# Performance work log

Hardware: AMD Instinct MI355X
Metric: run time of the kernel (lower is better)

## Reference

```python
import jax, jax.numpy as jnp
import numpy as np

EPS = 1e-12
W_MAX = 0.8
ALPHA_MAX = 1.5
T = 10
ETA = 0.2
ALPHA_SCALE = 1.0
N = 50000
IN_DIM = 512
HID = 256
C = 8
EH = 64
E2 = 400000  # undirected pairs; E = 2*E2 directed edges


def setup_inputs() -> dict:
    key = jax.random.key(0)
    ks = jax.random.split(key, 12)
    x = jax.random.normal(ks[0], (N, IN_DIM), jnp.float32)
    src0 = jax.random.randint(ks[1], (E2,), 0, N)
    dst0 = jax.random.randint(ks[2], (E2,), 0, N)
    edge_index = jnp.concatenate([jnp.stack([src0, dst0]), jnp.stack([dst0, src0])], axis=1)
    rev = jnp.concatenate([jnp.arange(E2) + E2, jnp.arange(E2)])
    def lin(k, i, o):
        return jax.random.normal(k, (i, o), jnp.float32) * (2.0 / i) ** 0.5
    enc_w1 = lin(ks[3], IN_DIM, HID); enc_b1 = jnp.zeros((HID,), jnp.float32)
    enc_w2 = lin(ks[4], HID, C); enc_b2 = jnp.zeros((C,), jnp.float32)
    edge_w1 = lin(ks[5], 2 * HID + 2, EH); edge_b1 = jnp.zeros((EH,), jnp.float32)
    edge_w2 = lin(ks[6], EH, 1); edge_b2 = jnp.zeros((1,), jnp.float32)
    bound = (6.0 / (C + C)) ** 0.5  # xavier_uniform
    R_raw = jax.random.uniform(ks[7], (C, C), jnp.float32, -bound, bound) + 0.5 * jnp.eye(C, dtype=jnp.float32)
    R_scale_log = jnp.float32(0.0)
    msg_logit = jnp.float32(-3.0)
    return dict(x=x, edge_index=edge_index, rev=rev,
                enc_w1=enc_w1, enc_b1=enc_b1, enc_w2=enc_w2, enc_b2=enc_b2,
                edge_w1=edge_w1, edge_b1=edge_b1, edge_w2=edge_w2, edge_b2=edge_b2,
                R_raw=R_raw, R_scale_log=R_scale_log, msg_logit=msg_logit)


def reference(x, edge_index, rev, enc_w1, enc_b1, enc_w2, enc_b2,
              edge_w1, edge_b1, edge_w2, edge_b2, R_raw, R_scale_log, msg_logit):
    num_nodes = x.shape[0]
    src, dst = edge_index[0], edge_index[1]
    # unary encoder (mlp type, eval mode -> no dropout)
    h = jax.nn.relu(x @ enc_w1 + enc_b1)
    logits = h @ enc_w2 + enc_b2
    log_phi = jax.nn.log_softmax(logits, axis=-1)  # [N, C]
    # structural edge features from out-degree of src
    deg = jax.ops.segment_sum(jnp.ones_like(src, jnp.float32), src, num_segments=num_nodes)
    logdeg = jnp.log(deg + 1.0)
    a, b = logdeg[src], logdeg[dst]
    struct = jnp.stack([a + b, jnp.abs(a - b)], axis=-1)  # [E, 2]
    # learned symmetric edge weights -> per-edge kernel K
    hs, hd = h[src], h[dst]
    edge_in = jnp.concatenate([hs * hd, jnp.abs(hs - hd), struct], axis=-1)  # [E, 2H+2]
    eh = jax.nn.relu(edge_in @ edge_w1 + edge_b1)
    w_raw = (eh @ edge_w2 + edge_b2)[:, 0]
    w = W_MAX * jax.nn.sigmoid(w_raw)
    w = 0.5 * (w + w[rev])
    R = 0.5 * (R_raw + R_raw.T)
    R = (jax.nn.softplus(R_scale_log) + 1e-06) * jnp.tanh(R)
    K = jnp.exp(w[:, None, None] * R[None])  # [E, C, C]
    degc = jnp.maximum(deg, 1.0)
    edge_norm = (degc[src] * degc[dst]) ** -0.5  # [E]
    alpha = ALPHA_MAX * jax.nn.sigmoid(msg_logit) * ALPHA_SCALE
    lp_src = log_phi[src]
    m = jax.nn.softmax(lp_src, axis=-1)  # init_unary=True

    def step(m, _):
        f = jnp.einsum('ec,ecd->ed', m, K)
        log_f = jnp.log(jnp.maximum(f, EPS)) * edge_norm[:, None]
        sum_in = jax.ops.segment_sum(log_f, dst, num_segments=num_nodes)
        excl = sum_in[src] - log_f[rev]
        m_new = jax.nn.softmax(lp_src + alpha * excl, axis=-1)
        m = (1.0 - ETA) * m + ETA * m_new
        m = jnp.maximum(m, EPS)
        m = m / m.sum(axis=-1, keepdims=True)
        return m, None

    m, _ = jax.lax.scan(step, m, None, length=T)
    # beliefs
    f = jnp.einsum('ec,ecd->ed', m, K)
    log_f = jnp.log(jnp.maximum(f, EPS)) * edge_norm[:, None]
    sum_in = jax.ops.segment_sum(log_f, dst, num_segments=num_nodes)
    beliefs = jax.nn.softmax(log_phi + alpha * sum_in, axis=-1)
    return beliefs
```

## Files before the change

kernel.cpp:

```cpp
#include <hip/hip_runtime.h>
#include <cstddef>
#include <cstdint>

typedef _Float16 h4 __attribute__((ext_vector_type(4)));
typedef _Float16 h8 __attribute__((ext_vector_type(8)));
typedef float    f4 __attribute__((ext_vector_type(4)));

#define NN      50000
#define IND     512
#define HIDN    256
#define E2P     400000
#define EDD     800000
#define NBLK    196

#define OFF_HF16    ((size_t)0)
#define OFF_LOGF    ((size_t)0)
#define OFF_Z       ((size_t)25600000)
#define OFF_DEG     ((size_t)28800000)
#define OFF_LOGDEG  ((size_t)29000000)
#define OFF_DEGC    ((size_t)29200000)
#define OFF_BASE    ((size_t)29400000)
#define OFF_CNT     ((size_t)29600000)
#define OFF_BLK     ((size_t)29800000)
#define OFF_WT      ((size_t)29804096)
#define OFF_BT      ((size_t)30066240)
#define OFF_RS      ((size_t)30135872)
#define OFF_WSYM    ((size_t)30136384)
#define OFF_ENORM   ((size_t)31736384)
#define OFF_POS     ((size_t)33336384)
#define OFF_MA      ((size_t)36536384)
#define OFF_MB      ((size_t)49336384)
#define WS_NEED     ((size_t)62136384)

__global__ void k_deg(const int* __restrict__ ei, int* __restrict__ deg) {
    int e = blockIdx.x * 256 + threadIdx.x;
    atomicAdd(&deg[ei[e]], 1);
}

__global__ void k_node(const int* __restrict__ deg, float* __restrict__ logdeg,
                       float* __restrict__ degc) {
    int n = blockIdx.x * 256 + threadIdx.x;
    if (n < NN) {
        float d = (float)deg[n];
        logdeg[n] = logf(d + 1.0f);
        degc[n]   = fmaxf(d, 1.0f);
    }
}

__global__ void k_scan1(const int* __restrict__ deg, int* __restrict__ incl,
                        int* __restrict__ blk) {
    __shared__ int sm[256];
    int i = blockIdx.x * 256 + threadIdx.x;
    int v = (i < NN) ? deg[i] : 0;
    sm[threadIdx.x] = v;
    __syncthreads();
    for (int off = 1; off < 256; off <<= 1) {
        int t = (threadIdx.x >= off) ? sm[threadIdx.x - off] : 0;
        __syncthreads();
        sm[threadIdx.x] += t;
        __syncthreads();
    }
    if (i < NN) incl[i] = sm[threadIdx.x];
    if (threadIdx.x == 255) blk[blockIdx.x] = sm[255];
}

__global__ void k_scan2(int* __restrict__ blk) {
    __shared__ int sm[256];
    int v = (threadIdx.x < NBLK) ? blk[threadIdx.x] : 0;
    sm[threadIdx.x] = v;
    __syncthreads();
    for (int off = 1; off < 256; off <<= 1) {
        int t = (threadIdx.x >= off) ? sm[threadIdx.x - off] : 0;
        __syncthreads();
        sm[threadIdx.x] += t;
        __syncthreads();
    }
    if (threadIdx.x < NBLK) blk[threadIdx.x] = sm[threadIdx.x];
}

__global__ void k_scan3(const int* __restrict__ incl, const int* __restrict__ deg,
                        const int* __restrict__ blk, int* __restrict__ base) {
    int i = blockIdx.x * 256 + threadIdx.x;
    if (i < NN) {
        int off = (blockIdx.x > 0) ? blk[blockIdx.x - 1] : 0;
        base[i] = off + incl[i] - deg[i];
    }
}

__global__ void k_pos(const int* __restrict__ ei, const int* __restrict__ base,
                      int* __restrict__ cnt, int* __restrict__ pos) {
    int e = blockIdx.x * 256 + threadIdx.x;
    int dstn = ei[EDD + e];
    pos[e] = base[dstn] + atomicAdd(&cnt[dstn], 1);
}

__global__ void k_prep(const float* __restrict__ enc_w1, const float* __restrict__ edge_w1,
                       const float* __restrict__ R_raw, const float* __restrict__ Rsl,
                       const float* __restrict__ mlog,
                       _Float16* __restrict__ Wt, _Float16* __restrict__ Bt,
                       float* __restrict__ Rs) {
    int gid = blockIdx.x * 256 + threadIdx.x;
    if (gid < 256 * 512) {
        int n = gid >> 9, k = gid & 511;
        Wt[n * 512 + k] = (_Float16)enc_w1[k * 256 + n];
        return;
    }
    int g2 = gid - 256 * 512;
    if (g2 < 64 * 544) {
        int n = g2 / 544, k = g2 - n * 544;
        float v = 0.0f;
        if (k < 512) {
            int tm = k >> 5, r = k & 31;
            int qq = r >> 3, jj = (r >> 1) & 3, typ = k & 1;
            int c = (tm >> 1) * 32 + qq * 8 + (tm & 1) * 4 + jj;
            v = edge_w1[(typ ? 256 + c : c) * 64 + n];
        } else if (k < 514) {
            v = edge_w1[k * 64 + n];
        }
        Bt[n * 544 + k] = (_Float16)v;
        return;
    }
    int g3 = g2 - 64 * 544;
    if (g3 < 64) {
        int c = g3 >> 3, d = g3 & 7;
        float rv = 0.5f * (R_raw[c * 8 + d] + R_raw[d * 8 + c]);
        float s  = log1pf(expf(Rsl[0])) + 1e-6f;
        Rs[g3] = s * tanhf(rv);
        return;
    }
    if (g3 == 64) {
        Rs[64] = 1.5f / (1.0f + expf(-mlog[0]));
    }
}

__global__ __launch_bounds__(256) void k_enc(const float* __restrict__ x,
                                             const _Float16* __restrict__ Wt,
                                             const float* __restrict__ b1,
                                             _Float16* __restrict__ hf) {
    __shared__ _Float16 XL[64 * 40];
    __shared__ _Float16 WL[256 * 40];
    const int tid = threadIdx.x;
    const int wid = tid >> 6;
    const int lane = tid & 63;
    const int l15 = lane & 15;
    const int q = lane >> 4;
    const int m0 = blockIdx.x * 64;

    f4 acc[16];
#pragma unroll
    for (int i = 0; i < 16; i++) acc[i] = (f4){0.f, 0.f, 0.f, 0.f};

    const int xr = tid >> 2;
    const int xs = tid & 3;
    const int gr = m0 + xr;

    for (int kt = 0; kt < 16; kt++) {
        __syncthreads();
        f4 xv0 = (f4){0, 0, 0, 0}, xv1 = (f4){0, 0, 0, 0};
        if (gr < NN) {
            const f4* xp = (const f4*)(x + (size_t)gr * IND + kt * 32 + xs * 8);
            xv0 = xp[0]; xv1 = xp[1];
        }
        h8 xh;
#pragma unroll
        for (int u = 0; u < 4; u++) { xh[u] = (_Float16)xv0[u]; xh[4 + u] = (_Float16)xv1[u]; }
        *(h8*)&XL[xr * 40 + xs * 8] = xh;
#pragma unroll
        for (int rep = 0; rep < 4; rep++) {
            int cid = rep * 256 + tid;
            int n = cid >> 2;
            int off = (cid & 3) * 8;
            h8 wv = *(const h8*)(Wt + (size_t)n * IND + kt * 32 + off);
            *(h8*)&WL[n * 40 + off] = wv;
        }
        __syncthreads();
        h8 a = *(const h8*)&XL[(wid * 16 + l15) * 40 + q * 8];
#pragma unroll
        for (int nt = 0; nt < 16; nt++) {
            h8 b = *(const h8*)&WL[(nt * 16 + l15) * 40 + q * 8];
            acc[nt] = __builtin_amdgcn_mfma_f32_16x16x32_f16(a, b, acc[nt], 0, 0, 0);
        }
    }
#pragma unroll
    for (int nt = 0; nt < 16; nt++) {
        int col = nt * 16 + l15;
        float bv = b1[col];
#pragma unroll
        for (int reg = 0; reg < 4; reg++) {
            int row = m0 + wid * 16 + q * 4 + reg;
            if (row < NN) {
                float v = acc[nt][reg] + bv;
                hf[(size_t)row * HIDN + col] = (_Float16)fmaxf(v, 0.f);
            }
        }
    }
}

__global__ void k_logits(const _Float16* __restrict__ hf, const float* __restrict__ w2,
                         const float* __restrict__ b2, float* __restrict__ Z) {
    __shared__ float w2L[2048];
    for (int i = threadIdx.x; i < 2048; i += 256) w2L[i] = w2[i];
    __syncthreads();
    int n = blockIdx.x * 256 + threadIdx.x;
    if (n >= NN) return;
    float sum[8];
#pragma unroll
    for (int c = 0; c < 8; c++) sum[c] = b2[c];
    for (int kb = 0; kb < 32; kb++) {
        h8 hv = *(const h8*)(hf + (size_t)n * HIDN + kb * 8);
#pragma unroll
        for (int u = 0; u < 8; u++) {
            float hx = (float)hv[u];
            const float* wr = &w2L[(kb * 8 + u) * 8];
#pragma unroll
            for (int c = 0; c < 8; c++) sum[c] += hx * wr[c];
        }
    }
    float mx = sum[0];
#pragma unroll
    for (int c = 1; c < 8; c++) mx = fmaxf(mx, sum[c]);
    float se = 0.f;
#pragma unroll
    for (int c = 0; c < 8; c++) se += __expf(sum[c] - mx);
    float lse = __logf(se);
#pragma unroll
    for (int c = 0; c < 8; c++) Z[(size_t)n * 16 + c] = sum[c] - mx - lse;
}

__global__ __launch_bounds__(256) void k_edge(const int* __restrict__ ei,
        const _Float16* __restrict__ hf, const float* __restrict__ logdeg,
        const _Float16* __restrict__ BtG, const float* __restrict__ eb1,
        const float* __restrict__ ew2, const float* __restrict__ eb2,
        float* __restrict__ wsym) {
    __shared__ _Float16 BtL[64 * 136];
    const int tid = threadIdx.x;
    const int wid = tid >> 6;
    const int lane = tid & 63;
    const int l15 = lane & 15;
    const int q = lane >> 4;
    const int eb = blockIdx.x * 256;

    int sidx[4], didx[4];
    float la[4], lb[4];
#pragma unroll
    for (int mt = 0; mt < 4; mt++) {
        int e = eb + wid * 64 + mt * 16 + l15;
        int ee = (e < E2P) ? e : 0;
        sidx[mt] = ei[ee];
        didx[mt] = ei[EDD + ee];
        la[mt] = logdeg[sidx[mt]];
        lb[mt] = logdeg[didx[mt]];
    }

    f4 acc[4][4];
#pragma unroll
    for (int a = 0; a < 4; a++)
#pragma unroll
        for (int b = 0; b < 4; b++) acc[a][b] = (f4){0.f, 0.f, 0.f, 0.f};

    const _Float16* hq = hf + q * 8;
    h8 curS[4], curD[4];
#pragma unroll
    for (int mt = 0; mt < 4; mt++) {
        curS[mt] = *(const h8*)(hq + (size_t)sidx[mt] * HIDN);
        curD[mt] = *(const h8*)(hq + (size_t)didx[mt] * HIDN);
    }

    for (int ph = 0; ph < 4; ph++) {
        __syncthreads();
        {
            const int r = tid & 63;
            const int cb = tid >> 6;
            const int kbase = ph * 128;
#pragma unroll
            for (int i = 0; i < 4; i++) {
                int ck = cb + i * 4;
                *(h8*)&BtL[r * 136 + ck * 8] =
                    *(const h8*)(BtG + (size_t)r * 544 + kbase + ck * 8);
            }
        }
        __syncthreads();
#pragma unroll
        for (int kk2 = 0; kk2 < 2; kk2++) {
            const int kk = ph * 2 + kk2;
            h8 nxtS[4], nxtD[4];
            if (kk < 7) {
                const int c1 = (kk + 1) * 32;
#pragma unroll
                for (int mt = 0; mt < 4; mt++) {
                    nxtS[mt] = *(const h8*)(hq + (size_t)sidx[mt] * HIDN + c1);
                    nxtD[mt] = *(const h8*)(hq + (size_t)didx[mt] * HIDN + c1);
                }
            }
            const int ko = kk2 * 64 + q * 8;
            {
                h8 a0[4];
#pragma unroll
                for (int mt = 0; mt < 4; mt++) {
#pragma unroll
                    for (int j = 0; j < 4; j++) {
                        float x1 = (float)curS[mt][j], x2 = (float)curD[mt][j];
                        a0[mt][2 * j]     = (_Float16)(x1 * x2);
                        a0[mt][2 * j + 1] = (_Float16)fabsf(x1 - x2);
                    }
                }
                h8 bf[4];
#pragma unroll
                for (int nt = 0; nt < 4; nt++)
                    bf[nt] = *(const h8*)&BtL[(nt * 16 + l15) * 136 + ko];
#pragma unroll
                for (int mt = 0; mt < 4; mt++)
#pragma unroll
                    for (int nt = 0; nt < 4; nt++)
                        acc[mt][nt] = __builtin_amdgcn_mfma_f32_16x16x32_f16(a0[mt], bf[nt], acc[mt][nt], 0, 0, 0);
            }
            {
                h8 a1[4];
#pragma unroll
                for (int mt = 0; mt < 4; mt++) {
#pragma unroll
                    for (int j = 0; j < 4; j++) {
                        float x1 = (float)curS[mt][4 + j], x2 = (float)curD[mt][4 + j];
                        a1[mt][2 * j]     = (_Float16)(x1 * x2);
                        a1[mt][2 * j + 1] = (_Float16)fabsf(x1 - x2);
                    }
                }
                h8 bf[4];
#pragma unroll
                for (int nt = 0; nt < 4; nt++)
                    bf[nt] = *(const h8*)&BtL[(nt * 16 + l15) * 136 + ko + 32];
#pragma unroll
                for (int mt = 0; mt < 4; mt++)
#pragma unroll
                    for (int nt = 0; nt < 4; nt++)
                        acc[mt][nt] = __builtin_amdgcn_mfma_f32_16x16x32_f16(a1[mt], bf[nt], acc[mt][nt], 0, 0, 0);
            }
            if (kk < 7) {
#pragma unroll
                for (int mt = 0; mt < 4; mt++) { curS[mt] = nxtS[mt]; curD[mt] = nxtD[mt]; }
            }
        }
    }

    __syncthreads();
    {
        const int r = tid & 63, ck = tid >> 6;
        *(h8*)&BtL[r * 136 + ck * 8] = *(const h8*)(BtG + (size_t)r * 544 + 512 + ck * 8);
    }
    __syncthreads();
    {
        h8 bf[4];
#pragma unroll
        for (int nt = 0; nt < 4; nt++)
            bf[nt] = *(const h8*)&BtL[(nt * 16 + l15) * 136 + q * 8];
#pragma unroll
        for (int mt = 0; mt < 4; mt++) {
            h8 a = (h8){0, 0, 0, 0, 0, 0, 0, 0};
            if (q == 0) {
                a[0] = (_Float16)(la[mt] + lb[mt]);
                a[1] = (_Float16)fabsf(la[mt] - lb[mt]);
            }
#pragma unroll
            for (int nt = 0; nt < 4; nt++)
                acc[mt][nt] = __builtin_amdgcn_mfma_f32_16x16x32_f16(a, bf[nt], acc[mt][nt], 0, 0, 0);
        }
    }

    float b1v[4], w2v[4];
#pragma unroll
    for (int nt = 0; nt < 4; nt++) {
        int col = nt * 16 + l15;
        b1v[nt] = eb1[col];
        w2v[nt] = ew2[col];
    }
    const float b2s = eb2[0];
    float part[4][4];
#pragma unroll
    for (int mt = 0; mt < 4; mt++)
#pragma unroll
        for (int reg = 0; reg < 4; reg++) {
            float s = 0.f;
#pragma unroll
            for (int nt = 0; nt < 4; nt++) {
                float v = acc[mt][nt][reg] + b1v[nt];
                s += fmaxf(v, 0.f) * w2v[nt];
            }
            part[mt][reg] = s;
        }
#pragma unroll
    for (int off = 1; off < 16; off <<= 1)
#pragma unroll
        for (int mt = 0; mt < 4; mt++)
#pragma unroll
            for (int reg = 0; reg < 4; reg++)
                part[mt][reg] += __shfl_xor(part[mt][reg], off, 64);
    if (l15 == 0) {
#pragma unroll
        for (int mt = 0; mt < 4; mt++)
#pragma unroll
            for (int reg = 0; reg < 4; reg++) {
                int er = eb + wid * 64 + mt * 16 + q * 4 + reg;
                if (er < E2P) {
                    float xr = part[mt][reg] + b2s;
                    wsym[er] = 0.8f / (1.0f + __expf(-xr));
                }
            }
    }
}


__global__ __launch_bounds__(256) void k_init(const int* __restrict__ ei,
        const float* __restrict__ wsymb, const float* __restrict__ degc,
        const float* __restrict__ Rs, const float* __restrict__ Z,
        const int* __restrict__ pos, _Float16* __restrict__ m,
        float* __restrict__ enorm, _Float16* __restrict__ logf) {
    __shared__ float RsL[64];
    const int tid = threadIdx.x;
    if (tid < 64) RsL[tid] = Rs[tid];
    __syncthreads();
    int p = blockIdx.x * 256 + tid;
    if (p >= E2P) return;
    int sp = ei[p], dp = ei[EDD + p];
    float w = wsymb[p];
    float nrm = rsqrtf(degc[sp] * degc[dp]);
    enorm[p] = nrm;
    const f4* Zs = (const f4*)(Z + (size_t)sp * 16);
    const f4* Zd = (const f4*)(Z + (size_t)dp * 16);
    f4 ls0 = Zs[0], ls1 = Zs[1], ld0 = Zd[0], ld1 = Zd[1];
    float lps[8], lpd[8];
#pragma unroll
    for (int u = 0; u < 4; u++) { lps[u] = ls0[u]; lps[4+u] = ls1[u]; lpd[u] = ld0[u]; lpd[4+u] = ld1[u]; }
    float me[8], mr[8];
    {
        float mx = lps[0], mx2 = lpd[0];
#pragma unroll
        for (int d = 1; d < 8; d++) { mx = fmaxf(mx, lps[d]); mx2 = fmaxf(mx2, lpd[d]); }
        float s = 0.f, s2 = 0.f;
#pragma unroll
        for (int d = 0; d < 8; d++) { me[d] = __expf(lps[d] - mx); s += me[d];
                                      mr[d] = __expf(lpd[d] - mx2); s2 += mr[d]; }
        float rs = 1.f / s, rs2 = 1.f / s2;
#pragma unroll
        for (int d = 0; d < 8; d++) { me[d] *= rs; mr[d] *= rs2; }
    }
    {
        h8 mh, mh2;
#pragma unroll
        for (int d = 0; d < 8; d++) { mh[d] = (_Float16)me[d]; mh2[d] = (_Float16)mr[d]; }
        *(h8*)(m + (size_t)p * 8) = mh;
        *(h8*)(m + (size_t)(E2P + p) * 8) = mh2;
    }
    float fe[8], fr[8];
#pragma unroll
    for (int d = 0; d < 8; d++) { fe[d] = 0.f; fr[d] = 0.f; }
#pragma unroll
    for (int c = 0; c < 8; c++) {
#pragma unroll
        for (int d = 0; d < 8; d++) {
            float kv = __expf(w * RsL[c * 8 + d]);
            fe[d] += me[c] * kv;
            fr[d] += mr[c] * kv;
        }
    }
    h8 le, lr;
#pragma unroll
    for (int d = 0; d < 8; d++) {
        le[d] = (_Float16)(__logf(fmaxf(fe[d], 1e-12f)) * nrm);
        lr[d] = (_Float16)(__logf(fmaxf(fr[d], 1e-12f)) * nrm);
    }
    *(h8*)(logf + (size_t)pos[p] * 8)       = le;
    *(h8*)(logf + (size_t)pos[E2P + p] * 8) = lr;
}

__global__ __launch_bounds__(256) void k_bpF(const int* __restrict__ ei,
        const float* __restrict__ wsymb, const float* __restrict__ enorm,
        const float* __restrict__ Rs, const float* __restrict__ Z,
        const int* __restrict__ pos, const _Float16* __restrict__ m,
        _Float16* __restrict__ mo, _Float16* __restrict__ logf) {
    __shared__ float RsL[64];
    const int tid = threadIdx.x;
    if (tid < 64) RsL[tid] = Rs[tid];
    __syncthreads();
    int p = blockIdx.x * 256 + tid;
    if (p >= E2P) return;
    int sp = ei[p], dp = ei[EDD + p];
    float w = wsymb[p], nrm = enorm[p];
    const float alpha = Rs[64];
    h8 mhe = *(const h8*)(m + (size_t)p * 8);
    h8 mhr = *(const h8*)(m + (size_t)(E2P + p) * 8);
    float me[8], mr[8];
#pragma unroll
    for (int d = 0; d < 8; d++) { me[d] = (float)mhe[d]; mr[d] = (float)mhr[d]; }
    float fe[8], fr[8];
#pragma unroll
    for (int d = 0; d < 8; d++) { fe[d] = 0.f; fr[d] = 0.f; }
#pragma unroll
    for (int c = 0; c < 8; c++) {
#pragma unroll
        for (int d = 0; d < 8; d++) {
            float kv = __expf(w * RsL[c * 8 + d]);
            fe[d] += me[c] * kv;
            fr[d] += mr[c] * kv;
        }
    }
    float lfe[8], lfr[8];
#pragma unroll
    for (int d = 0; d < 8; d++) {
        lfe[d] = __logf(fmaxf(fe[d], 1e-12f)) * nrm;
        lfr[d] = __logf(fmaxf(fr[d], 1e-12f)) * nrm;
    }
    const f4* Zs = (const f4*)(Z + (size_t)sp * 16);
    const f4* Zd = (const f4*)(Z + (size_t)dp * 16);
    f4 ls0 = Zs[0], ls1 = Zs[1], ss0 = Zs[2], ss1 = Zs[3];
    f4 ld0 = Zd[0], ld1 = Zd[1], sd0 = Zd[2], sd1 = Zd[3];
    float te[8], tr[8];
#pragma unroll
    for (int u = 0; u < 4; u++) {
        te[u]     = ls0[u] + alpha * (ss0[u] - lfr[u]);
        te[4 + u] = ls1[u] + alpha * (ss1[u] - lfr[4 + u]);
        tr[u]     = ld0[u] + alpha * (sd0[u] - lfe[u]);
        tr[4 + u] = ld1[u] + alpha * (sd1[u] - lfe[4 + u]);
    }
    float m1[8], m2[8];
    {
        float mx = te[0], mx2 = tr[0];
#pragma unroll
        for (int d = 1; d < 8; d++) { mx = fmaxf(mx, te[d]); mx2 = fmaxf(mx2, tr[d]); }
        float s = 0.f, s2 = 0.f;
#pragma unroll
        for (int d = 0; d < 8; d++) { m1[d] = __expf(te[d] - mx); s += m1[d];
                                      m2[d] = __expf(tr[d] - mx2); s2 += m2[d]; }
        float rs = 1.f / s, rs2 = 1.f / s2;
        float t1 = 0.f, t2 = 0.f;
#pragma unroll
        for (int d = 0; d < 8; d++) {
            m1[d] = fmaxf(0.8f * me[d] + 0.2f * m1[d] * rs, 1e-12f);  t1 += m1[d];
            m2[d] = fmaxf(0.8f * mr[d] + 0.2f * m2[d] * rs2, 1e-12f); t2 += m2[d];
        }
        float rt1 = 1.f / t1, rt2 = 1.f / t2;
#pragma unroll
        for (int d = 0; d < 8; d++) { m1[d] *= rt1; m2[d] *= rt2; }
    }
    {
        h8 mh, mh2;
#pragma unroll
        for (int d = 0; d < 8; d++) { mh[d] = (_Float16)m1[d]; mh2[d] = (_Float16)m2[d]; }
        *(h8*)(mo + (size_t)p * 8) = mh;
        *(h8*)(mo + (size_t)(E2P + p) * 8) = mh2;
    }
    float fe2[8], fr2[8];
#pragma unroll
    for (int d = 0; d < 8; d++) { fe2[d] = 0.f; fr2[d] = 0.f; }
#pragma unroll
    for (int c = 0; c < 8; c++) {
#pragma unroll
        for (int d = 0; d < 8; d++) {
            float kv = __expf(w * RsL[c * 8 + d]);
            fe2[d] += m1[c] * kv;
            fr2[d] += m2[c] * kv;
        }
    }
    h8 le, lr;
#pragma unroll
    for (int d = 0; d < 8; d++) {
        le[d] = (_Float16)(__logf(fmaxf(fe2[d], 1e-12f)) * nrm);
        lr[d] = (_Float16)(__logf(fmaxf(fr2[d], 1e-12f)) * nrm);
    }
    *(h8*)(logf + (size_t)pos[p] * 8)       = le;
    *(h8*)(logf + (size_t)pos[E2P + p] * 8) = lr;
}

__global__ void k_sum(const _Float16* __restrict__ logf, const int* __restrict__ base,
                      const int* __restrict__ deg, float* __restrict__ Z) {
    int g = blockIdx.x * 256 + threadIdx.x;
    int n = g >> 3;
    if (n >= NN) return;
    int j = threadIdx.x & 7;
    int b = base[n], cnt = deg[n];
    float acc[8];
#pragma unroll
    for (int d = 0; d < 8; d++) acc[d] = 0.f;
    for (int s = j; s < cnt; s += 8) {
        h8 v = *(const h8*)(logf + (size_t)(b + s) * 8);
#pragma unroll
        for (int d = 0; d < 8; d++) acc[d] += (float)v[d];
    }
    int lane = threadIdx.x & 63;
    float v4[4], v2[2], r;
    {
        bool hi = (lane & 4) != 0;
#pragma unroll
        for (int i = 0; i < 4; i++) {
            float send = hi ? acc[i] : acc[i + 4];
            float recv = __shfl_xor(send, 4, 64);
            v4[i] = (hi ? acc[i + 4] : acc[i]) + recv;
        }
    }
    {
        bool hi = (lane & 2) != 0;
#pragma unroll
        for (int i = 0; i < 2; i++) {
            float send = hi ? v4[i] : v4[i + 2];
            float recv = __shfl_xor(send, 2, 64);
            v2[i] = (hi ? v4[i + 2] : v4[i]) + recv;
        }
    }
    {
        bool hi = (lane & 1) != 0;
        float send = hi ? v2[0] : v2[1];
        float recv = __shfl_xor(send, 1, 64);
        r = (hi ? v2[1] : v2[0]) + recv;
    }
    Z[(size_t)n * 16 + 8 + j] = r;
}

__global__ void k_bel(const float* __restrict__ Z, const float* __restrict__ Rs,
                      float* __restrict__ out) {
    int tid = blockIdx.x * 256 + threadIdx.x;
    if (tid >= NN * 8) return;
    int n = tid >> 3, d = tid & 7;
    float alpha = Rs[64];
    float v = Z[(size_t)n * 16 + d] + alpha * Z[(size_t)n * 16 + 8 + d];
    float mx = v;
    mx = fmaxf(mx, __shfl_xor(mx, 1, 64));
    mx = fmaxf(mx, __shfl_xor(mx, 2, 64));
    mx = fmaxf(mx, __shfl_xor(mx, 4, 64));
    float ex = __expf(v - mx);
    float s = ex;
    s += __shfl_xor(s, 1, 64); s += __shfl_xor(s, 2, 64); s += __shfl_xor(s, 4, 64);
    out[tid] = ex / s;
}

extern "C" void kernel_launch(void* const* d_in, const int* in_sizes, int n_in,
                              void* d_out, int out_size, void* d_ws, size_t ws_size,
                              hipStream_t stream) {
    if (ws_size < WS_NEED) return;
    const float* x        = (const float*)d_in[0];
    const int*   ei       = (const int*)d_in[1];
    const float* enc_w1   = (const float*)d_in[3];
    const float* enc_b1   = (const float*)d_in[4];
    const float* enc_w2   = (const float*)d_in[5];
    const float* enc_b2   = (const float*)d_in[6];
    const float* edge_w1  = (const float*)d_in[7];
    const float* edge_b1  = (const float*)d_in[8];
    const float* edge_w2  = (const float*)d_in[9];
    const float* edge_b2  = (const float*)d_in[10];
    const float* R_raw    = (const float*)d_in[11];
    const float* Rsl      = (const float*)d_in[12];
    const float* mlog     = (const float*)d_in[13];

    char* ws = (char*)d_ws;
    _Float16* hf     = (_Float16*)(ws + OFF_HF16);
    _Float16* logfb  = (_Float16*)(ws + OFF_LOGF);
    float* Zb        = (float*)(ws + OFF_Z);
    int*   deg       = (int*)  (ws + OFF_DEG);
    float* logdeg    = (float*)(ws + OFF_LOGDEG);
    float* degc      = (float*)(ws + OFF_DEGC);
    int*   baseA     = (int*)  (ws + OFF_BASE);
    int*   cnt       = (int*)  (ws + OFF_CNT);
    int*   blk       = (int*)  (ws + OFF_BLK);
    _Float16* Wt     = (_Float16*)(ws + OFF_WT);
    _Float16* Bt     = (_Float16*)(ws + OFF_BT);
    float* Rs        = (float*)(ws + OFF_RS);
    float* wsym      = (float*)(ws + OFF_WSYM);
    float* enorm     = (float*)(ws + OFF_ENORM);
    int*   pos       = (int*)  (ws + OFF_POS);
    _Float16* mA     = (_Float16*)(ws + OFF_MA);
    _Float16* mB     = (_Float16*)(ws + OFF_MB);

    hipMemsetAsync(deg, 0, (size_t)NN * 4, stream);
    k_deg<<<dim3(EDD / 256), dim3(256), 0, stream>>>(ei, deg);
    k_node<<<dim3(NBLK), dim3(256), 0, stream>>>(deg, logdeg, degc);
    k_prep<<<dim3((256 * 512 + 64 * 544 + 65 + 255) / 256), dim3(256), 0, stream>>>(
        enc_w1, edge_w1, R_raw, Rsl, mlog, Wt, Bt, Rs);
    k_scan1<<<dim3(NBLK), dim3(256), 0, stream>>>(deg, cnt , blk);
    k_scan2<<<dim3(1), dim3(256), 0, stream>>>(blk);
    k_scan3<<<dim3(NBLK), dim3(256), 0, stream>>>(cnt, deg, blk, baseA);
    hipMemsetAsync(cnt, 0, (size_t)NN * 4, stream);
    k_pos<<<dim3(EDD / 256), dim3(256), 0, stream>>>(ei, baseA, cnt, pos);
    k_enc<<<dim3((NN + 63) / 64), dim3(256), 0, stream>>>(x, Wt, enc_b1, hf);
    k_logits<<<dim3(NBLK), dim3(256), 0, stream>>>(hf, enc_w2, enc_b2, Zb);
    k_edge<<<dim3((E2P + 255) / 256), dim3(256), 0, stream>>>(ei, hf, logdeg, Bt, edge_b1,
                                                              edge_w2, edge_b2, wsym);
    k_init<<<dim3((E2P + 255) / 256), dim3(256), 0, stream>>>(ei, wsym, degc, Rs, Zb,
                                                              pos, mA, enorm, logfb);
    k_sum<<<dim3((NN * 8 + 255) / 256), dim3(256), 0, stream>>>(logfb, baseA, deg, Zb);
    _Float16* mc = mA; _Float16* mn = mB;
    for (int t = 0; t < 10; t++) {
        k_bpF<<<dim3((E2P + 255) / 256), dim3(256), 0, stream>>>(ei, wsym, enorm, Rs,
                                                                 Zb, pos, mc, mn, logfb);
        k_sum<<<dim3((NN * 8 + 255) / 256), dim3(256), 0, stream>>>(logfb, baseA, deg, Zb);
        _Float16* tm = mc; mc = mn; mn = tm;
    }
    k_bel<<<dim3((NN * 8 + 255) / 256), dim3(256), 0, stream>>>(Zb, Rs, (float*)d_out);
    (void)in_sizes; (void)n_in; (void)out_size;
}
```

Measured before the change: 835.3 us.

## Sort edge pairs by source, pack per-edge metadata, exploit kernel symmetry, fuse beliefs

Undirected edge pairs are reordered by source node through a counting sort, so the Z gathers in the BP loop get more locality. Per-edge indices, weight and norm are packed into i4/float2 arrays so each thread does coalesced loads, and both directions' messages are interleaved in one in-place buffer. The symmetric R matrix halves the exp calls in the K-product, and the final belief softmax is fused into the last k_sum. The edge MLP kernel also drops to 128 edges per block. In exchange there are extra preprocessing launches and atomics, and messages are now updated in place.

Measured after the change: 798.7 us. 1.05x faster.

```diff
diff --git a/kernel.cpp b/kernel.cpp
--- a/kernel.cpp
+++ b/kernel.cpp
@@ -5,6 +5,7 @@
 typedef _Float16 h4 __attribute__((ext_vector_type(4)));
 typedef _Float16 h8 __attribute__((ext_vector_type(8)));
 typedef float    f4 __attribute__((ext_vector_type(4)));
+typedef int      i4 __attribute__((ext_vector_type(4)));
 
 #define NN      50000
 #define IND     512
@@ -12,6 +13,7 @@
 #define E2P     400000
 #define EDD     800000
 #define NBLK    196
+#define EBLK    1563
 
 #define OFF_HF16    ((size_t)0)
 #define OFF_LOGF    ((size_t)0)
@@ -26,11 +28,14 @@
 #define OFF_BT      ((size_t)30066240)
 #define OFF_RS      ((size_t)30135872)
 #define OFF_WSYM    ((size_t)30136384)
-#define OFF_ENORM   ((size_t)31736384)
-#define OFF_POS     ((size_t)33336384)
-#define OFF_MA      ((size_t)36536384)
-#define OFF_MB      ((size_t)49336384)
-#define WS_NEED     ((size_t)62136384)
+#define OFF_POS     ((size_t)31736384)
+#define OFF_ORDER   ((size_t)34936384)
+#define OFF_BASE2   ((size_t)36536384)
+#define OFF_OFS2    ((size_t)36736384)
+#define OFF_PRC     ((size_t)36936384)
+#define OFF_WN      ((size_t)43336384)
+#define OFF_M       ((size_t)46536384)
+#define WS_NEED     ((size_t)59336384)
 
 __global__ void k_deg(const int* __restrict__ ei, int* __restrict__ deg) {
     int e = blockIdx.x * 256 + threadIdx.x;
@@ -94,6 +99,20 @@
     pos[e] = base[dstn] + atomicAdd(&cnt[dstn], 1);
 }
 
+__global__ void k_cnt2(const int* __restrict__ ei, int* __restrict__ cnt2) {
+    int p = blockIdx.x * 256 + threadIdx.x;
+    if (p < E2P) atomicAdd(&cnt2[ei[p]], 1);
+}
+
+__global__ void k_order(const int* __restrict__ ei, const int* __restrict__ base2,
+                        int* __restrict__ ofs2, int* __restrict__ order) {
+    int p = blockIdx.x * 256 + threadIdx.x;
+    if (p < E2P) {
+        int s = ei[p];
+        order[base2[s] + atomicAdd(&ofs2[s], 1)] = p;
+    }
+}
+
 __global__ void k_prep(const float* __restrict__ enc_w1, const float* __restrict__ edge_w1,
                        const float* __restrict__ R_raw, const float* __restrict__ Rsl,
                        const float* __restrict__ mlog,
@@ -238,30 +257,29 @@
     const int lane = tid & 63;
     const int l15 = lane & 15;
     const int q = lane >> 4;
-    const int eb = blockIdx.x * 256;
-
-    int sidx[4], didx[4];
-    float la[4], lb[4];
-#pragma unroll
-    for (int mt = 0; mt < 4; mt++) {
-        int e = eb + wid * 64 + mt * 16 + l15;
-        int ee = (e < E2P) ? e : 0;
-        sidx[mt] = ei[ee];
-        didx[mt] = ei[EDD + ee];
+    const int eb = blockIdx.x * 128;
+
+    int sidx[2], didx[2];
+    float la[2], lb[2];
+#pragma unroll
+    for (int mt = 0; mt < 2; mt++) {
+        int e = eb + wid * 32 + mt * 16 + l15;
+        sidx[mt] = ei[e];
+        didx[mt] = ei[EDD + e];
         la[mt] = logdeg[sidx[mt]];
         lb[mt] = logdeg[didx[mt]];
     }
 
-    f4 acc[4][4];
-#pragma unroll
-    for (int a = 0; a < 4; a++)
+    f4 acc[2][4];
+#pragma unroll
+    for (int a = 0; a < 2; a++)
 #pragma unroll
         for (int b = 0; b < 4; b++) acc[a][b] = (f4){0.f, 0.f, 0.f, 0.f};
 
     const _Float16* hq = hf + q * 8;
-    h8 curS[4], curD[4];
-#pragma unroll
-    for (int mt = 0; mt < 4; mt++) {
+    h8 curS[2], curD[2];
+#pragma unroll
+    for (int mt = 0; mt < 2; mt++) {
         curS[mt] = *(const h8*)(hq + (size_t)sidx[mt] * HIDN);
         curD[mt] = *(const h8*)(hq + (size_t)didx[mt] * HIDN);
     }
@@ -283,20 +301,20 @@
 #pragma unroll
         for (int kk2 = 0; kk2 < 2; kk2++) {
             const int kk = ph * 2 + kk2;
-            h8 nxtS[4], nxtD[4];
+            h8 nxtS[2], nxtD[2];
             if (kk < 7) {
                 const int c1 = (kk + 1) * 32;
 #pragma unroll
-                for (int mt = 0; mt < 4; mt++) {
+                for (int mt = 0; mt < 2; mt++) {
                     nxtS[mt] = *(const h8*)(hq + (size_t)sidx[mt] * HIDN + c1);
                     nxtD[mt] = *(const h8*)(hq + (size_t)didx[mt] * HIDN + c1);
                 }
             }
             const int ko = kk2 * 64 + q * 8;
             {
-                h8 a0[4];
-#pragma unroll
-                for (int mt = 0; mt < 4; mt++) {
+                h8 a0[2];
+#pragma unroll
+                for (int mt = 0; mt < 2; mt++) {
 #pragma unroll
                     for (int j = 0; j < 4; j++) {
                         float x1 = (float)curS[mt][j], x2 = (float)curD[mt][j];
@@ -309,15 +327,15 @@
                 for (int nt = 0; nt < 4; nt++)
                     bf[nt] = *(const h8*)&BtL[(nt * 16 + l15) * 136 + ko];
 #pragma unroll
-                for (int mt = 0; mt < 4; mt++)
+                for (int mt = 0; mt < 2; mt++)
 #pragma unroll
                     for (int nt = 0; nt < 4; nt++)
                         acc[mt][nt] = __builtin_amdgcn_mfma_f32_16x16x32_f16(a0[mt], bf[nt], acc[mt][nt], 0, 0, 0);
             }
             {
-                h8 a1[4];
-#pragma unroll
-                for (int mt = 0; mt < 4; mt++) {
+                h8 a1[2];
+#pragma unroll
+                for (int mt = 0; mt < 2; mt++) {
 #pragma unroll
                     for (int j = 0; j < 4; j++) {
                         float x1 = (float)curS[mt][4 + j], x2 = (float)curD[mt][4 + j];
@@ -330,14 +348,14 @@
                 for (int nt = 0; nt < 4; nt++)
                     bf[nt] = *(const h8*)&BtL[(nt * 16 + l15) * 136 + ko + 32];
 #pragma unroll
-                for (int mt = 0; mt < 4; mt++)
+                for (int mt = 0; mt < 2; mt++)
 #pragma unroll
                     for (int nt = 0; nt < 4; nt++)
                         acc[mt][nt] = __builtin_amdgcn_mfma_f32_16x16x32_f16(a1[mt], bf[nt], acc[mt][nt], 0, 0, 0);
             }
             if (kk < 7) {
 #pragma unroll
-                for (int mt = 0; mt < 4; mt++) { curS[mt] = nxtS[mt]; curD[mt] = nxtD[mt]; }
+                for (int mt = 0; mt < 2; mt++) { curS[mt] = nxtS[mt]; curD[mt] = nxtD[mt]; }
             }
         }
     }
@@ -354,7 +372,7 @@
         for (int nt = 0; nt < 4; nt++)
             bf[nt] = *(const h8*)&BtL[(nt * 16 + l15) * 136 + q * 8];
 #pragma unroll
-        for (int mt = 0; mt < 4; mt++) {
+        for (int mt = 0; mt < 2; mt++) {
             h8 a = (h8){0, 0, 0, 0, 0, 0, 0, 0};
             if (q == 0) {
                 a[0] = (_Float16)(la[mt] + lb[mt]);
@@ -374,9 +392,9 @@
         w2v[nt] = ew2[col];
     }
     const float b2s = eb2[0];
-    float part[4][4];
-#pragma unroll
-    for (int mt = 0; mt < 4; mt++)
+    float part[2][4];
+#pragma unroll
+    for (int mt = 0; mt < 2; mt++)
 #pragma unroll
         for (int reg = 0; reg < 4; reg++) {
             float s = 0.f;
@@ -390,16 +408,16 @@
 #pragma unroll
     for (int off = 1; off < 16; off <<= 1)
 #pragma unroll
-        for (int mt = 0; mt < 4; mt++)
+        for (int mt = 0; mt < 2; mt++)
 #pragma unroll
             for (int reg = 0; reg < 4; reg++)
                 part[mt][reg] += __shfl_xor(part[mt][reg], off, 64);
     if (l15 == 0) {
 #pragma unroll
-        for (int mt = 0; mt < 4; mt++)
+        for (int mt = 0; mt < 2; mt++)
 #pragma unroll
             for (int reg = 0; reg < 4; reg++) {
-                int er = eb + wid * 64 + mt * 16 + q * 4 + reg;
+                int er = eb + wid * 32 + mt * 16 + q * 4 + reg;
                 if (er < E2P) {
                     float xr = part[mt][reg] + b2s;
                     wsym[er] = 0.8f / (1.0f + __expf(-xr));
@@ -409,21 +427,46 @@
 }
 
 
+__device__ __forceinline__ void kprod(const float* __restrict__ RsL, float w,
+                                      const float* me, const float* mr,
+                                      float* fe, float* fr) {
+#pragma unroll
+    for (int d = 0; d < 8; d++) { fe[d] = 0.f; fr[d] = 0.f; }
+#pragma unroll
+    for (int c = 0; c < 8; c++) {
+        {
+            float kv = __expf(w * RsL[c * 8 + c]);
+            fe[c] += me[c] * kv;
+            fr[c] += mr[c] * kv;
+        }
+#pragma unroll
+        for (int d = c + 1; d < 8; d++) {
+            float kv = __expf(w * RsL[c * 8 + d]);
+            fe[d] += me[c] * kv; fr[d] += mr[c] * kv;
+            fe[c] += me[d] * kv; fr[c] += mr[d] * kv;
+        }
+    }
+}
+
 __global__ __launch_bounds__(256) void k_init(const int* __restrict__ ei,
         const float* __restrict__ wsymb, const float* __restrict__ degc,
         const float* __restrict__ Rs, const float* __restrict__ Z,
-        const int* __restrict__ pos, _Float16* __restrict__ m,
-        float* __restrict__ enorm, _Float16* __restrict__ logf) {
+        const int* __restrict__ pos, const int* __restrict__ order,
+        i4* __restrict__ prc, float2* __restrict__ wn,
+        _Float16* __restrict__ M, _Float16* __restrict__ logf) {
     __shared__ float RsL[64];
     const int tid = threadIdx.x;
     if (tid < 64) RsL[tid] = Rs[tid];
     __syncthreads();
-    int p = blockIdx.x * 256 + tid;
-    if (p >= E2P) return;
+    int i = blockIdx.x * 256 + tid;
+    if (i >= E2P) return;
+    int p = order[i];
     int sp = ei[p], dp = ei[EDD + p];
     float w = wsymb[p];
     float nrm = rsqrtf(degc[sp] * degc[dp]);
-    enorm[p] = nrm;
+    int pz0 = pos[p], pz1 = pos[E2P + p];
+    prc[i] = (i4){sp, dp, pz0, pz1};
+    wn[i] = make_float2(w, nrm);
     const f4* Zs = (const f4*)(Z + (size_t)sp * 16);
     const f4* Zd = (const f4*)(Z + (size_t)dp * 16);
     f4 ls0 = Zs[0], ls1 = Zs[1], ld0 = Zd[0], ld1 = Zd[1];
@@ -447,62 +490,43 @@
         h8 mh, mh2;
 #pragma unroll
         for (int d = 0; d < 8; d++) { mh[d] = (_Float16)me[d]; mh2[d] = (_Float16)mr[d]; }
-        *(h8*)(m + (size_t)p * 8) = mh;
-        *(h8*)(m + (size_t)(E2P + p) * 8) = mh2;
+        *(h8*)(M + (size_t)i * 16)     = mh;
+        *(h8*)(M + (size_t)i * 16 + 8) = mh2;
     }
     float fe[8], fr[8];
-#pragma unroll
-    for (int d = 0; d < 8; d++) { fe[d] = 0.f; fr[d] = 0.f; }
-#pragma unroll
-    for (int c = 0; c < 8; c++) {
-#pragma unroll
-        for (int d = 0; d < 8; d++) {
-            float kv = __expf(w * RsL[c * 8 + d]);
-            fe[d] += me[c] * kv;
-            fr[d] += mr[c] * kv;
-        }
-    }
+    kprod(RsL, w, me, mr, fe, fr);
     h8 le, lr;
 #pragma unroll
     for (int d = 0; d < 8; d++) {
         le[d] = (_Float16)(__logf(fmaxf(fe[d], 1e-12f)) * nrm);
         lr[d] = (_Float16)(__logf(fmaxf(fr[d], 1e-12f)) * nrm);
     }
-    *(h8*)(logf + (size_t)pos[p] * 8)       = le;
-    *(h8*)(logf + (size_t)pos[E2P + p] * 8) = lr;
-}
-
-__global__ __launch_bounds__(256) void k_bpF(const int* __restrict__ ei,
-        const float* __restrict__ wsymb, const float* __restrict__ enorm,
-        const float* __restrict__ Rs, const float* __restrict__ Z,
-        const int* __restrict__ pos, const _Float16* __restrict__ m,
-        _Float16* __restrict__ mo, _Float16* __restrict__ logf) {
+    *(h8*)(logf + (size_t)pz0 * 8) = le;
+    *(h8*)(logf + (size_t)pz1 * 8) = lr;
+}
+
+__global__ __launch_bounds__(256) void k_bpF(const i4* __restrict__ prc,
+        const float2* __restrict__ wn, const float* __restrict__ Rs,
+        const float* __restrict__ Z, _Float16* __restrict__ M,
+        _Float16* __restrict__ logf) {
     __shared__ float RsL[64];
     const int tid = threadIdx.x;
     if (tid < 64) RsL[tid] = Rs[tid];
     __syncthreads();
-    int p = blockIdx.x * 256 + tid;
-    if (p >= E2P) return;
-    int sp = ei[p], dp = ei[EDD + p];
-    float w = wsymb[p], nrm = enorm[p];
+    int i = blockIdx.x * 256 + tid;
+    if (i >= E2P) return;
+    i4 c4 = prc[i];
+    const int sp = c4[0], dp = c4[1], pz0 = c4[2], pz1 = c4[3];
+    float2 wnv = wn[i];
+    const float w = wnv.x, nrm = wnv.y;
     const float alpha = Rs[64];
-    h8 mhe = *(const h8*)(m + (size_t)p * 8);
-    h8 mhr = *(const h8*)(m + (size_t)(E2P + p) * 8);
+    h8 mhe = *(const h8*)(M + (size_t)i * 16);
+    h8 mhr = *(const h8*)(M + (size_t)i * 16 + 8);
     float me[8], mr[8];
 #pragma unroll
     for (int d = 0; d < 8; d++) { me[d] = (float)mhe[d]; mr[d] = (float)mhr[d]; }
     float fe[8], fr[8];
-#pragma unroll
-    for (int d = 0; d < 8; d++) { fe[d] = 0.f; fr[d] = 0.f; }
-#pragma unroll
-    for (int c = 0; c < 8; c++) {
-#pragma unroll
-        for (int d = 0; d < 8; d++) {
-            float kv = __expf(w * RsL[c * 8 + d]);
-            fe[d] += me[c] * kv;
-            fr[d] += mr[c] * kv;
-        }
-    }
+    kprod(RsL, w, me, mr, fe, fr);
     float lfe[8], lfr[8];
 #pragma unroll
     for (int d = 0; d < 8; d++) {
@@ -545,33 +569,24 @@
         h8 mh, mh2;
 #pragma unroll
         for (int d = 0; d < 8; d++) { mh[d] = (_Float16)m1[d]; mh2[d] = (_Float16)m2[d]; }
-        *(h8*)(mo + (size_t)p * 8) = mh;
-        *(h8*)(mo + (size_t)(E2P + p) * 8) = mh2;
+        *(h8*)(M + (size_t)i * 16)     = mh;
+        *(h8*)(M + (size_t)i * 16 + 8) = mh2;
     }
     float fe2[8], fr2[8];
-#pragma unroll
-    for (int d = 0; d < 8; d++) { fe2[d] = 0.f; fr2[d] = 0.f; }
-#pragma unroll
-    for (int c = 0; c < 8; c++) {
-#pragma unroll
-        for (int d = 0; d < 8; d++) {
-            float kv = __expf(w * RsL[c * 8 + d]);
-            fe2[d] += m1[c] * kv;
-            fr2[d] += m2[c] * kv;
-        }
-    }
+    kprod(RsL, w, m1, m2, fe2, fr2);
     h8 le, lr;
 #pragma unroll
     for (int d = 0; d < 8; d++) {
         le[d] = (_Float16)(__logf(fmaxf(fe2[d], 1e-12f)) * nrm);
         lr[d] = (_Float16)(__logf(fmaxf(fr2[d], 1e-12f)) * nrm);
     }
-    *(h8*)(logf + (size_t)pos[p] * 8)       = le;
-    *(h8*)(logf + (size_t)pos[E2P + p] * 8) = lr;
+    *(h8*)(logf + (size_t)pz0 * 8) = le;
+    *(h8*)(logf + (size_t)pz1 * 8) = lr;
 }
 
 __global__ void k_sum(const _Float16* __restrict__ logf, const int* __restrict__ base,
-                      const int* __restrict__ deg, float* __restrict__ Z) {
+                      const int* __restrict__ deg, float* __restrict__ Z,
+                      const float* __restrict__ Rs, float* __restrict__ out, int fin) {
     int g = blockIdx.x * 256 + threadIdx.x;
     int n = g >> 3;
     if (n >= NN) return;
@@ -611,24 +626,20 @@
         float recv = __shfl_xor(send, 1, 64);
         r = (hi ? v2[1] : v2[0]) + recv;
     }
-    Z[(size_t)n * 16 + 8 + j] = r;
-}
-
-__global__ void k_bel(const float* __restrict__ Z, const float* __restrict__ Rs,
-                      float* __restrict__ out) {
-    int tid = blockIdx.x * 256 + threadIdx.x;
-    if (tid >= NN * 8) return;
-    int n = tid >> 3, d = tid & 7;
-    float alpha = Rs[64];
-    float v = Z[(size_t)n * 16 + d] + alpha * Z[(size_t)n * 16 + 8 + d];
-    float mx = v;
-    mx = fmaxf(mx, __shfl_xor(mx, 1, 64));
-    mx = fmaxf(mx, __shfl_xor(mx, 2, 64));
-    mx = fmaxf(mx, __shfl_xor(mx, 4, 64));
-    float ex = __expf(v - mx);
-    float s = ex;
-    s += __shfl_xor(s, 1, 64); s += __shfl_xor(s, 2, 64); s += __shfl_xor(s, 4, 64);
-    out[tid] = ex / s;
+    if (!fin) {
+        Z[(size_t)n * 16 + 8 + j] = r;
+    } else {
+        float alpha = Rs[64];
+        float v = Z[(size_t)n * 16 + j] + alpha * r;
+        float mx = v;
+        mx = fmaxf(mx, __shfl_xor(mx, 1, 64));
+        mx = fmaxf(mx, __shfl_xor(mx, 2, 64));
+        mx = fmaxf(mx, __shfl_xor(mx, 4, 64));
+        float ex = __expf(v - mx);
+        float s = ex;
+        s += __shfl_xor(s, 1, 64); s += __shfl_xor(s, 2, 64); s += __shfl_xor(s, 4, 64);
+        out[(size_t)n * 8 + j] = ex / s;
+    }
 }
 
 extern "C" void kernel_launch(void* const* d_in, const int* in_sizes, int n_in,
@@ -663,10 +674,14 @@
     _Float16* Bt     = (_Float16*)(ws + OFF_BT);
     float* Rs        = (float*)(ws + OFF_RS);
     float* wsym      = (float*)(ws + OFF_WSYM);
-    float* enorm     = (float*)(ws + OFF_ENORM);
     int*   pos       = (int*)  (ws + OFF_POS);
-    _Float16* mA     = (_Float16*)(ws + OFF_MA);
-    _Float16* mB     = (_Float16*)(ws + OFF_MB);
+    int*   order     = (int*)  (ws + OFF_ORDER);
+    int*   base2     = (int*)  (ws + OFF_BASE2);
+    int*   ofs2      = (int*)  (ws + OFF_OFS2);
+    i4*    prc       = (i4*)   (ws + OFF_PRC);
+    float2* wnb      = (float2*)(ws + OFF_WN);
+    _Float16* Mb     = (_Float16*)(ws + OFF_M);
+    float* outp      = (float*)d_out;
 
     hipMemsetAsync(deg, 0, (size_t)NN * 4, stream);
     k_deg<<<dim3(EDD / 256), dim3(256), 0, stream>>>(ei, deg);
@@ -678,20 +693,25 @@
     k_scan3<<<dim3(NBLK), dim3(256), 0, stream>>>(cnt, deg, blk, baseA);
     hipMemsetAsync(cnt, 0, (size_t)NN * 4, stream);
     k_pos<<<dim3(EDD / 256), dim3(256), 0, stream>>>(ei, baseA, cnt, pos);
+    hipMemsetAsync(ofs2, 0, (size_t)NN * 4, stream);
+    k_cnt2<<<dim3(EBLK), dim3(256), 0, stream>>>(ei, ofs2);
+    k_scan1<<<dim3(NBLK), dim3(256), 0, stream>>>(ofs2, cnt, blk);
+    k_scan2<<<dim3(1), dim3(256), 0, stream>>>(blk);
+    k_scan3<<<dim3(NBLK), dim3(256), 0, stream>>>(cnt, ofs2, blk, base2);
+    hipMemsetAsync(ofs2, 0, (size_t)NN * 4, stream);
+    k_order<<<dim3(EBLK), dim3(256), 0, stream>>>(ei, base2, ofs2, order);
     k_enc<<<dim3((NN + 63) / 64), dim3(256), 0, stream>>>(x, Wt, enc_b1, hf);
     k_logits<<<dim3(NBLK), dim3(256), 0, stream>>>(hf, enc_w2, enc_b2, Zb);
-    k_edge<<<dim3((E2P + 255) / 256), dim3(256), 0, stream>>>(ei, hf, logdeg, Bt, edge_b1,
-                                                              edge_w2, edge_b2, wsym);
-    k_init<<<dim3((E2P + 255) / 256), dim3(256), 0, stream>>>(ei, wsym, degc, Rs, Zb,
-                                                              pos, mA, enorm, logfb);
-    k_sum<<<dim3((NN * 8 + 255) / 256), dim3(256), 0, stream>>>(logfb, baseA, deg, Zb);
-    _Float16* mc = mA; _Float16* mn = mB;
+    k_edge<<<dim3(E2P / 128), dim3(256), 0, stream>>>(ei, hf, logdeg, Bt, edge_b1,
+                                                      edge_w2, edge_b2, wsym);
+    k_init<<<dim3(EBLK), dim3(256), 0, stream>>>(ei, wsym, degc, Rs, Zb, pos, order,
+                                                 prc, wnb, Mb, logfb);
+    k_sum<<<dim3((NN * 8 + 255) / 256), dim3(256), 0, stream>>>(logfb, baseA, deg, Zb,
+                                                                Rs, outp, 0);
     for (int t = 0; t < 10; t++) {
-        k_bpF<<<dim3((E2P + 255) / 256), dim3(256), 0, stream>>>(ei, wsym, enorm, Rs,
-                                                                 Zb, pos, mc, mn, logfb);
-        k_sum<<<dim3((NN * 8 + 255) / 256), dim3(256), 0, stream>>>(logfb, baseA, deg, Zb);
-        _Float16* tm = mc; mc = mn; mn = tm;
-    }
-    k_bel<<<dim3((NN * 8 + 255) / 256), dim3(256), 0, stream>>>(Zb, Rs, (float*)d_out);
+        k_bpF<<<dim3(EBLK), dim3(256), 0, stream>>>(prc, wnb, Rs, Zb, Mb, logfb);
+        k_sum<<<dim3((NN * 8 + 255) / 256), dim3(256), 0, stream>>>(logfb, baseA, deg, Zb,
+                                                                    Rs, outp, (t == 9) ? 1 : 0);
+    }
     (void)in_sizes; (void)n_in; (void)out_size;
 }
```
